# Kernel optimization log

Hardware: AMD Instinct MI355X
Metric: run time of the kernel (lower is better)

## Reference

```python
import jax, jax.numpy as jnp
import numpy as np
from jax import lax

EPS = 1e-5
B = 512

def _conv(x, w, pad):
    # x: [B,Cin,H,W], w: [Cout,Cin,kh,kw]
    return lax.conv_general_dilated(x, w, (1, 1), [(pad, pad), (pad, pad)],
                                    dimension_numbers=('NCHW', 'OIHW', 'NCHW'))

def _bn2d(x, g, b, m, v):
    s = g * lax.rsqrt(v + EPS)
    return x * s[None, :, None, None] + (b - m * s)[None, :, None, None]

def _bn1d(x, g, b, m, v):
    s = g * lax.rsqrt(v + EPS)
    return x * s + (b - m * s)

def _pool2(x):
    return lax.reduce_window(x, -jnp.inf, lax.max, (1, 1, 2, 2), (1, 1, 2, 2), 'VALID')

def setup_inputs() -> dict:
    key = jax.random.key(0)
    ks = iter(jax.random.split(key, 64))
    rn = lambda shape, s=1.0: jax.random.normal(next(ks), shape, dtype=jnp.float32) * s
    un = lambda shape: jax.random.uniform(next(ks), shape, dtype=jnp.float32, minval=0.5, maxval=1.5)
    def bn_params(c):
        return (jnp.ones((c,), jnp.float32), jnp.zeros((c,), jnp.float32), rn((c,), 0.1), un((c,)))
    inp = {"x": rn((B, 3, 64, 64))}
    inp["w1"] = rn((32, 3, 5, 5), 0.1)
    inp["bn1_g"], inp["bn1_b"], inp["bn1_m"], inp["bn1_v"] = bn_params(32)
    inp["w2"] = rn((64, 32, 3, 3), 0.06)
    inp["bn2_g"], inp["bn2_b"], inp["bn2_m"], inp["bn2_v"] = bn_params(64)
    inp["w3"] = rn((128, 64, 3, 3), 0.04)
    inp["bn3_g"], inp["bn3_b"], inp["bn3_m"], inp["bn3_v"] = bn_params(128)
    inp["fc_w"] = rn((256, 8192), 0.01)
    inp["fc_b"] = jnp.zeros((256,), jnp.float32)
    inp["bnf_g"], inp["bnf_b"], inp["bnf_m"], inp["bnf_v"] = bn_params(256)
    inp["c_w1"] = rn((64, 256), 0.06)
    inp["c_b1"] = jnp.zeros((64,), jnp.float32)
    inp["bnc_g"], inp["bnc_b"], inp["bnc_m"], inp["bnc_v"] = bn_params(64)
    inp["c_w2"] = rn((1, 64), 0.1)
    inp["c_b2"] = jnp.zeros((1,), jnp.float32)
    inp["m_w1"] = rn((64, 256), 0.06)
    inp["m_b1"] = jnp.zeros((64,), jnp.float32)
    inp["bnm_g"], inp["bnm_b"], inp["bnm_m"], inp["bnm_v"] = bn_params(64)
    inp["m_w2"] = rn((1, 64), 0.1)
    inp["m_b2"] = jnp.zeros((1,), jnp.float32)
    return inp

def reference(x, w1, bn1_g, bn1_b, bn1_m, bn1_v,
              w2, bn2_g, bn2_b, bn2_m, bn2_v,
              w3, bn3_g, bn3_b, bn3_m, bn3_v,
              fc_w, fc_b, bnf_g, bnf_b, bnf_m, bnf_v,
              c_w1, c_b1, bnc_g, bnc_b, bnc_m, bnc_v, c_w2, c_b2,
              m_w1, m_b1, bnm_g, bnm_b, bnm_m, bnm_v, m_w2, m_b2):
    # Block 1: conv5x5(3->32) + BN + ReLU + maxpool2 -> [B,32,32,32]
    h = _pool2(jax.nn.relu(_bn2d(_conv(x, w1, 2), bn1_g, bn1_b, bn1_m, bn1_v)))
    # Block 2: conv3x3(32->64) + BN + ReLU + maxpool2 -> [B,64,16,16]
    h = _pool2(jax.nn.relu(_bn2d(_conv(h, w2, 1), bn2_g, bn2_b, bn2_m, bn2_v)))
    # Block 3: conv3x3(64->128) + BN + ReLU + maxpool2 + ToDense -> [B,128,8,8]
    h = _pool2(jax.nn.relu(_bn2d(_conv(h, w3, 1), bn3_g, bn3_b, bn3_m, bn3_v)))
    f = h.reshape(h.shape[0], -1)  # [B, 8192]
    s = jax.nn.relu(_bn1d(f @ fc_w.T + fc_b, bnf_g, bnf_b, bnf_m, bnf_v))  # [B,256]
    c = jax.nn.relu(_bn1d(s @ c_w1.T + c_b1, bnc_g, bnc_b, bnc_m, bnc_v)) @ c_w2.T + c_b2
    mo = jax.nn.relu(_bn1d(s @ m_w1.T + m_b1, bnm_g, bnm_b, bnm_m, bnm_v)) @ m_w2.T + m_b2
    return (c, mo)  # ([B,1], [B,1])
```

## Files before the change

### kernel.cpp

```cpp
#include <hip/hip_runtime.h>
#include <hip/hip_bf16.h>

#define EPS 1e-5f

typedef __attribute__((ext_vector_type(8))) short bf16x8;
typedef __attribute__((ext_vector_type(4))) float f32x4;

__device__ __forceinline__ ushort f2b(float f) {
    return __builtin_bit_cast(ushort, __float2bfloat16(f));
}
__device__ __forceinline__ bf16x8 ld_frag(const char* p) {
    return __builtin_bit_cast(bf16x8, *reinterpret_cast<const uint4*>(p));
}

__global__ __launch_bounds__(256) void k_prep(
    const float* __restrict__ w1, const float* __restrict__ w2,
    const float* __restrict__ w3, const float* __restrict__ fcw,
    ushort* __restrict__ w1p, ushort* __restrict__ w2p,
    ushort* __restrict__ w3p, ushort* __restrict__ fcwp)
{
    const int total = 5120 + 18432 + 73728 + 2097152;
    for (int i = blockIdx.x * 256 + threadIdx.x; i < total; i += gridDim.x * 256) {
        if (i < 5120) {
            const int ky = i >> 10, co = (i >> 5) & 31, k = i & 31;
            const int kx = k >> 2, ci = k & 3;
            float v = 0.f;
            if (kx < 5 && ci < 3) v = w1[((co * 3 + ci) * 5 + ky) * 5 + kx];
            w1p[i] = f2b(v);
        } else if (i < 5120 + 18432) {
            const int j = i - 5120;
            const int tap = j >> 11, co = (j >> 5) & 63, ci = j & 31;
            w2p[j] = f2b(w2[(co * 32 + ci) * 9 + tap]);
        } else if (i < 5120 + 18432 + 73728) {
            const int j = i - (5120 + 18432);
            const int tap = j >> 13, co = (j >> 6) & 127, ci = j & 63;
            w3p[j] = f2b(w3[(co * 64 + ci) * 9 + tap]);
        } else {
            const int j = i - (5120 + 18432 + 73728);
            const int jrow = j >> 13, kp = j & 8191;
            const int c = kp & 127, p = kp >> 7;
            fcwp[j] = f2b(fcw[jrow * 8192 + c * 64 + p]);
        }
    }
}

__global__ __launch_bounds__(256) void k_conv1(
    const float* __restrict__ x, const ushort* __restrict__ w1p,
    const float* __restrict__ bg, const float* __restrict__ bb,
    const float* __restrict__ bm, const float* __restrict__ bv,
    ushort* __restrict__ h1)
{
    __shared__ __align__(16) ushort xs[12 * 72 * 4];
    __shared__ __align__(16) ushort ws[5 * 32 * 32];
    const int bid = blockIdx.x;
    const int n = bid >> 3, q = bid & 7;
    const int t = threadIdx.x;
    const int wave = t >> 6, lane = t & 63;
    const int g = lane >> 4, l15 = lane & 15;

    for (int idx = t; idx < 864; idx += 256) {
        const int row = idx / 72, col = idx - row * 72;
        const int gr = 8 * q - 2 + row, gc = col - 2;
        ushort p0 = 0, p1 = 0, p2 = 0;
        if ((unsigned)gr < 64u && (unsigned)gc < 64u) {
            const size_t base = ((size_t)n * 3 << 12) + (gr << 6) + gc;
            p0 = f2b(x[base]); p1 = f2b(x[base + 4096]); p2 = f2b(x[base + 8192]);
        }
        ushort4 pk; pk.x = p0; pk.y = p1; pk.z = p2; pk.w = 0;
        *reinterpret_cast<ushort4*>(&xs[idx * 4]) = pk;
    }
    for (int i = t; i < 640; i += 256) {
        const int gg = i & 3, r = i >> 2;
        const int co = r & 31;
        const uint4 v = *reinterpret_cast<const uint4*>(&w1p[r * 32 + gg * 8]);
        *reinterpret_cast<uint4*>((char*)ws + r * 64 + ((gg ^ ((co >> 1) & 3)) << 4)) = v;
    }
    __syncthreads();

    f32x4 acc[8][2];
    #pragma unroll
    for (int i = 0; i < 8; ++i) { acc[i][0] = (f32x4){0,0,0,0}; acc[i][1] = (f32x4){0,0,0,0}; }

    const char* xsb = (const char*)xs;
    const char* wsb = (const char*)ws;
    #pragma unroll
    for (int ky = 0; ky < 5; ++ky) {
        bf16x8 a[8], b[2];
        #pragma unroll
        for (int mt = 0; mt < 8; ++mt) {
            const int crl = 2 * wave + (mt >> 2);
            const int ccl = (mt & 3) * 16 + l15;
            const int off = ((crl + ky) * 72 + ccl) * 8 + g * 16;
            const uint2 lo = *reinterpret_cast<const uint2*>(xsb + off);
            const uint2 hi = *reinterpret_cast<const uint2*>(xsb + off + 8);
            uint4 all; all.x = lo.x; all.y = lo.y; all.z = hi.x; all.w = hi.y;
            a[mt] = __builtin_bit_cast(bf16x8, all);
        }
        #pragma unroll
        for (int nt = 0; nt < 2; ++nt) {
            const int co = nt * 16 + l15;
            b[nt] = ld_frag(wsb + (ky * 32 + co) * 64 + ((g ^ ((co >> 1) & 3)) << 4));
        }
        #pragma unroll
        for (int mt = 0; mt < 8; ++mt)
            #pragma unroll
            for (int nt = 0; nt < 2; ++nt)
                acc[mt][nt] = __builtin_amdgcn_mfma_f32_16x16x32_bf16(a[mt], b[nt], acc[mt][nt], 0, 0, 0);
    }

    const int prow = q * 4 + wave;
    #pragma unroll
    for (int nt = 0; nt < 2; ++nt) {
        const int co = nt * 16 + l15;
        const float s = bg[co] * rsqrtf(bv[co] + EPS);
        const float bsv = bb[co] - bm[co] * s;
        #pragma unroll
        for (int mt = 0; mt < 4; ++mt) {
            #pragma unroll
            for (int j = 0; j < 2; ++j) {
                const float v0 = fmaxf(fmaf(acc[mt][nt][2 * j],     s, bsv), 0.f);
                const float v1 = fmaxf(fmaf(acc[mt][nt][2 * j + 1], s, bsv), 0.f);
                const float v2 = fmaxf(fmaf(acc[mt + 4][nt][2 * j],     s, bsv), 0.f);
                const float v3 = fmaxf(fmaf(acc[mt + 4][nt][2 * j + 1], s, bsv), 0.f);
                const int ppc = mt * 8 + g * 2 + j;
                h1[(((size_t)n * 32 + prow) * 32 + ppc) * 32 + co] =
                    f2b(fmaxf(fmaxf(v0, v1), fmaxf(v2, v3)));
            }
        }
    }
}

__global__ __launch_bounds__(256) void k_conv2(
    const ushort* __restrict__ h1, const ushort* __restrict__ w2p,
    const float* __restrict__ bg, const float* __restrict__ bb,
    const float* __restrict__ bm, const float* __restrict__ bv,
    ushort* __restrict__ h2)
{
    __shared__ __align__(16) ushort xs[10 * 34 * 32];
    __shared__ __align__(16) ushort ws[9 * 64 * 32];
    const int bid = blockIdx.x;
    const int n = bid >> 2, q = bid & 3;
    const int t = threadIdx.x;
    const int wave = t >> 6, lane = t & 63;
    const int g = lane >> 4, l15 = lane & 15;

    for (int i = t; i < 1360; i += 256) {
        const int gg = i & 3, pix = i >> 2;
        const int row = pix / 34, col = pix - row * 34;
        const int gr = 8 * q - 1 + row, gc = col - 1;
        uint4 v = {0, 0, 0, 0};
        if ((unsigned)gr < 32u && (unsigned)gc < 32u)
            v = *reinterpret_cast<const uint4*>(&h1[((((size_t)n * 32 + gr) * 32 + gc) << 5) + gg * 8]);
        *reinterpret_cast<uint4*>((char*)xs + pix * 64 + ((gg ^ ((pix >> 1) & 3)) << 4)) = v;
    }
    for (int i = t; i < 2304; i += 256) {
        const int gg = i & 3, r = i >> 2;
        const int co = r & 63;
        const uint4 v = *reinterpret_cast<const uint4*>(&w2p[r * 32 + gg * 8]);
        *reinterpret_cast<uint4*>((char*)ws + r * 64 + ((gg ^ ((co >> 1) & 3)) << 4)) = v;
    }
    __syncthreads();

    f32x4 acc[4][4];
    #pragma unroll
    for (int i = 0; i < 4; ++i)
        #pragma unroll
        for (int j = 0; j < 4; ++j) acc[i][j] = (f32x4){0,0,0,0};

    const char* xsb = (const char*)xs;
    const char* wsb = (const char*)ws;
    #pragma unroll
    for (int tap = 0; tap < 9; ++tap) {
        const int ky = tap / 3, kx = tap - 3 * ky;
        bf16x8 a[4], b[4];
        #pragma unroll
        for (int mt = 0; mt < 4; ++mt) {
            const int crl = 2 * wave + (mt >> 1);
            const int ccl = (mt & 1) * 16 + l15;
            const int pix = (crl + ky) * 34 + ccl + kx;
            a[mt] = ld_frag(xsb + pix * 64 + ((g ^ ((pix >> 1) & 3)) << 4));
        }
        #pragma unroll
        for (int nt = 0; nt < 4; ++nt) {
            const int co = nt * 16 + l15;
            b[nt] = ld_frag(wsb + (tap * 64 + co) * 64 + ((g ^ ((co >> 1) & 3)) << 4));
        }
        #pragma unroll
        for (int mt = 0; mt < 4; ++mt)
            #pragma unroll
            for (int nt = 0; nt < 4; ++nt)
                acc[mt][nt] = __builtin_amdgcn_mfma_f32_16x16x32_bf16(a[mt], b[nt], acc[mt][nt], 0, 0, 0);
    }
    __syncthreads();

    const int prow = q * 4 + wave;
    #pragma unroll
    for (int nt = 0; nt < 4; ++nt) {
        const int co = nt * 16 + l15;
        const float s = bg[co] * rsqrtf(bv[co] + EPS);
        const float bsv = bb[co] - bm[co] * s;
        #pragma unroll
        for (int mtl = 0; mtl < 2; ++mtl) {
            #pragma unroll
            for (int j = 0; j < 2; ++j) {
                const float v0 = fmaxf(fmaf(acc[mtl][nt][2 * j],     s, bsv), 0.f);
                const float v1 = fmaxf(fmaf(acc[mtl][nt][2 * j + 1], s, bsv), 0.f);
                const float v2 = fmaxf(fmaf(acc[mtl + 2][nt][2 * j],     s, bsv), 0.f);
                const float v3 = fmaxf(fmaf(acc[mtl + 2][nt][2 * j + 1], s, bsv), 0.f);
                const int ppc = mtl * 8 + g * 2 + j;
                h2[(((size_t)n * 16 + prow) * 16 + ppc) * 64 + co] =
                    f2b(fmaxf(fmaxf(v0, v1), fmaxf(v2, v3)));
            }
        }
    }
}

__global__ __launch_bounds__(256) void k_conv3(
    const ushort* __restrict__ h2, const ushort* __restrict__ w3p,
    const float* __restrict__ bg, const float* __restrict__ bb,
    const float* __restrict__ bm, const float* __restrict__ bv,
    ushort* __restrict__ h3)
{
    __shared__ __align__(16) ushort xs[18 * 18 * 32];
    __shared__ __align__(16) ushort ws[9 * 64 * 32];
    const int bid = blockIdx.x;
    const int n = bid >> 1, ch = bid & 1;
    const int t = threadIdx.x;
    const int wave = t >> 6, lane = t & 63;
    const int g = lane >> 4, l15 = lane & 15;

    f32x4 acc[4][4];
    #pragma unroll
    for (int i = 0; i < 4; ++i)
        #pragma unroll
        for (int j = 0; j < 4; ++j) acc[i][j] = (f32x4){0,0,0,0};

    const char* xsb = (const char*)xs;
    const char* wsb = (const char*)ws;

    for (int gci = 0; gci < 2; ++gci) {
        if (gci) __syncthreads();
        for (int i = t; i < 1296; i += 256) {
            const int gg = i & 3, pix = i >> 2;
            const int row = pix / 18, col = pix - row * 18;
            const int gr = row - 1, gc = col - 1;
            uint4 v = {0, 0, 0, 0};
            if ((unsigned)gr < 16u && (unsigned)gc < 16u)
                v = *reinterpret_cast<const uint4*>(
                    &h2[((((size_t)n * 16 + gr) * 16 + gc) << 6) + gci * 32 + gg * 8]);
            *reinterpret_cast<uint4*>((char*)xs + pix * 64 + ((gg ^ ((pix >> 1) & 3)) << 4)) = v;
        }
        for (int i = t; i < 2304; i += 256) {
            const int gg = i & 3, r = i >> 2;
            const int tap = r >> 6, co = r & 63;
            const uint4 v = *reinterpret_cast<const uint4*>(
                &w3p[((size_t)(tap * 128 + ch * 64 + co) << 6) + gci * 32 + gg * 8]);
            *reinterpret_cast<uint4*>((char*)ws + r * 64 + ((gg ^ ((co >> 1) & 3)) << 4)) = v;
        }
        __syncthreads();
        #pragma unroll
        for (int tap = 0; tap < 9; ++tap) {
            const int ky = tap / 3, kx = tap - 3 * ky;
            bf16x8 a[4], b[4];
            #pragma unroll
            for (int mt = 0; mt < 4; ++mt) {
                const int pr = 4 * wave + mt;
                const int pix = (pr + ky) * 18 + l15 + kx;
                a[mt] = ld_frag(xsb + pix * 64 + ((g ^ ((pix >> 1) & 3)) << 4));
            }
            #pragma unroll
            for (int nt = 0; nt < 4; ++nt) {
                const int co = nt * 16 + l15;
                b[nt] = ld_frag(wsb + (tap * 64 + co) * 64 + ((g ^ ((co >> 1) & 3)) << 4));
            }
            #pragma unroll
            for (int mt = 0; mt < 4; ++mt)
                #pragma unroll
                for (int nt = 0; nt < 4; ++nt)
                    acc[mt][nt] = __builtin_amdgcn_mfma_f32_16x16x32_bf16(a[mt], b[nt], acc[mt][nt], 0, 0, 0);
        }
    }

    #pragma unroll
    for (int nt = 0; nt < 4; ++nt) {
        const int co = ch * 64 + nt * 16 + l15;
        const float s = bg[co] * rsqrtf(bv[co] + EPS);
        const float bsv = bb[co] - bm[co] * s;
        #pragma unroll
        for (int mtl = 0; mtl < 2; ++mtl) {
            #pragma unroll
            for (int j = 0; j < 2; ++j) {
                const int mt = mtl * 2;
                const float v0 = fmaxf(fmaf(acc[mt][nt][2 * j],     s, bsv), 0.f);
                const float v1 = fmaxf(fmaf(acc[mt][nt][2 * j + 1], s, bsv), 0.f);
                const float v2 = fmaxf(fmaf(acc[mt + 1][nt][2 * j],     s, bsv), 0.f);
                const float v3 = fmaxf(fmaf(acc[mt + 1][nt][2 * j + 1], s, bsv), 0.f);
                const int ppr = 2 * wave + mtl;
                const int ppc = g * 2 + j;
                h3[(((size_t)n * 8 + ppr) * 8 + ppc) * 128 + co] =
                    f2b(fmaxf(fmaxf(v0, v1), fmaxf(v2, v3)));
            }
        }
    }
}

__global__ __launch_bounds__(512) void k_fc(
    const ushort* __restrict__ A, const ushort* __restrict__ Bw, float* __restrict__ C)
{
    __shared__ __align__(16) ushort As[256 * 32];
    __shared__ __align__(16) ushort Bs[128 * 32];
    const int bm = blockIdx.x, bn = blockIdx.y, kz = blockIdx.z;
    const int t = threadIdx.x;
    const int wave = t >> 6, lane = t & 63;
    const int wm = wave >> 1, wn = wave & 1;
    const int g = lane >> 4, l15 = lane & 15;

    f32x4 acc[4][4];
    #pragma unroll
    for (int i = 0; i < 4; ++i)
        #pragma unroll
        for (int j = 0; j < 4; ++j) acc[i][j] = (f32x4){0,0,0,0};

    const char* asb = (const char*)As;
    const char* bsb = (const char*)Bs;
    for (int kk = 0; kk < 32; ++kk) {
        const int k0 = kz * 1024 + kk * 32;
        if (kk) __syncthreads();
        for (int i = t; i < 1536; i += 512) {
            const int gg = i & 3, row = (i >> 2);
            if (row < 256) {
                const uint4 v = *reinterpret_cast<const uint4*>(
                    &A[(size_t)(bm * 256 + row) * 8192 + k0 + gg * 8]);
                *reinterpret_cast<uint4*>((char*)As + row * 64 + ((gg ^ ((row >> 1) & 3)) << 4)) = v;
            } else {
                const int rw = row - 256;
                const uint4 v = *reinterpret_cast<const uint4*>(
                    &Bw[(size_t)(bn * 128 + rw) * 8192 + k0 + gg * 8]);
                *reinterpret_cast<uint4*>((char*)Bs + rw * 64 + ((gg ^ ((rw >> 1) & 3)) << 4)) = v;
            }
        }
        __syncthreads();
        bf16x8 a[4], b[4];
        #pragma unroll
        for (int mt = 0; mt < 4; ++mt) {
            const int r = wm * 64 + mt * 16 + l15;
            a[mt] = ld_frag(asb + r * 64 + ((g ^ ((r >> 1) & 3)) << 4));
        }
        #pragma unroll
        for (int nt = 0; nt < 4; ++nt) {
            const int r = wn * 64 + nt * 16 + l15;
            b[nt] = ld_frag(bsb + r * 64 + ((g ^ ((r >> 1) & 3)) << 4));
        }
        #pragma unroll
        for (int mt = 0; mt < 4; ++mt)
            #pragma unroll
            for (int nt = 0; nt < 4; ++nt)
                acc[mt][nt] = __builtin_amdgcn_mfma_f32_16x16x32_bf16(a[mt], b[nt], acc[mt][nt], 0, 0, 0);
    }

    #pragma unroll
    for (int mt = 0; mt < 4; ++mt) {
        #pragma unroll
        for (int nt = 0; nt < 4; ++nt) {
            const int col = bn * 128 + wn * 64 + nt * 16 + l15;
            #pragma unroll
            for (int r = 0; r < 4; ++r) {
                const int row = bm * 256 + wm * 64 + mt * 16 + g * 4 + r;
                atomicAdd(&C[(size_t)row * 256 + col], acc[mt][nt][r]);
            }
        }
    }
}

__global__ __launch_bounds__(128) void k_heads(
    const float* __restrict__ sraw, const float* __restrict__ fcb,
    const float* __restrict__ fg, const float* __restrict__ fb,
    const float* __restrict__ fm, const float* __restrict__ fv,
    const float* __restrict__ cw1, const float* __restrict__ cb1,
    const float* __restrict__ cg, const float* __restrict__ cbb,
    const float* __restrict__ cm, const float* __restrict__ cv,
    const float* __restrict__ cw2, const float* __restrict__ cb2,
    const float* __restrict__ mw1, const float* __restrict__ mb1,
    const float* __restrict__ mg, const float* __restrict__ mbb,
    const float* __restrict__ mm, const float* __restrict__ mv,
    const float* __restrict__ mw2, const float* __restrict__ mb2,
    float* __restrict__ outp)
{
    __shared__ float sv[256];
    const int b = blockIdx.x, t = threadIdx.x;
    for (int k = t; k < 256; k += 128) {
        const float val = sraw[b * 256 + k] + fcb[k];
        const float s = fg[k] * rsqrtf(fv[k] + EPS);
        sv[k] = fmaxf(fmaf(val, s, fb[k] - fm[k] * s), 0.f);
    }
    __syncthreads();
    const int j = t & 63;
    const bool isM = (t >= 64);
    const float* w1  = isM ? mw1 : cw1;
    const float* b1  = isM ? mb1 : cb1;
    const float* g1  = isM ? mg  : cg;
    const float* bb1 = isM ? mbb : cbb;
    const float* m1  = isM ? mm  : cm;
    const float* v1  = isM ? mv  : cv;
    const float* w2  = isM ? mw2 : cw2;
    const float* b2  = isM ? mb2 : cb2;
    float d = 0.f;
    const float* wr = w1 + j * 256;
    #pragma unroll 8
    for (int k = 0; k < 256; ++k) d = fmaf(sv[k], wr[k], d);
    d += b1[j];
    const float s1 = g1[j] * rsqrtf(v1[j] + EPS);
    d = fmaxf(fmaf(d, s1, bb1[j] - m1[j] * s1), 0.f);
    float prod = d * w2[j];
    #pragma unroll
    for (int off = 32; off > 0; off >>= 1) prod += __shfl_down(prod, off);
    if (j == 0) outp[(isM ? 512 : 0) + b] = prod + b2[0];
}

extern "C" void kernel_launch(void* const* d_in, const int* in_sizes, int n_in,
                              void* d_out, int out_size, void* d_ws, size_t ws_size,
                              hipStream_t stream)
{
    const float* x    = (const float*)d_in[0];
    const float* w1   = (const float*)d_in[1];
    const float* bn1g = (const float*)d_in[2];
    const float* bn1b = (const float*)d_in[3];
    const float* bn1m = (const float*)d_in[4];
    const float* bn1v = (const float*)d_in[5];
    const float* w2   = (const float*)d_in[6];
    const float* bn2g = (const float*)d_in[7];
    const float* bn2b = (const float*)d_in[8];
    const float* bn2m = (const float*)d_in[9];
    const float* bn2v = (const float*)d_in[10];
    const float* w3   = (const float*)d_in[11];
    const float* bn3g = (const float*)d_in[12];
    const float* bn3b = (const float*)d_in[13];
    const float* bn3m = (const float*)d_in[14];
    const float* bn3v = (const float*)d_in[15];
    const float* fcw  = (const float*)d_in[16];
    const float* fcb  = (const float*)d_in[17];
    const float* bnfg = (const float*)d_in[18];
    const float* bnfb = (const float*)d_in[19];
    const float* bnfm = (const float*)d_in[20];
    const float* bnfv = (const float*)d_in[21];
    const float* cw1  = (const float*)d_in[22];
    const float* cb1  = (const float*)d_in[23];
    const float* bncg = (const float*)d_in[24];
    const float* bncb = (const float*)d_in[25];
    const float* bncm = (const float*)d_in[26];
    const float* bncv = (const float*)d_in[27];
    const float* cw2  = (const float*)d_in[28];
    const float* cb2  = (const float*)d_in[29];
    const float* mw1  = (const float*)d_in[30];
    const float* mb1  = (const float*)d_in[31];
    const float* bnmg = (const float*)d_in[32];
    const float* bnmb = (const float*)d_in[33];
    const float* bnmm = (const float*)d_in[34];
    const float* bnmv = (const float*)d_in[35];
    const float* mw2  = (const float*)d_in[36];
    const float* mb2  = (const float*)d_in[37];

    char* W = (char*)d_ws;
    ushort* h1   = (ushort*)(W);
    ushort* h2   = (ushort*)(W + 33554432);
    ushort* h3   = (ushort*)(W + 50331648);
    float*  sr   = (float*) (W + 58720256);
    ushort* w1p  = (ushort*)(W + 59244544);
    ushort* w2p  = (ushort*)(W + 59254784);
    ushort* w3p  = (ushort*)(W + 59291648);
    ushort* fcwp = (ushort*)(W + 59439104);
    float* outp = (float*)d_out;

    k_prep<<<2048, 256, 0, stream>>>(w1, w2, w3, fcw, w1p, w2p, w3p, fcwp);
    k_conv1<<<512 * 8, 256, 0, stream>>>(x, w1p, bn1g, bn1b, bn1m, bn1v, h1);
    k_conv2<<<512 * 4, 256, 0, stream>>>(h1, w2p, bn2g, bn2b, bn2m, bn2v, h2);
    k_conv3<<<512 * 2, 256, 0, stream>>>(h2, w3p, bn3g, bn3b, bn3m, bn3v, h3);
    hipMemsetAsync(sr, 0, (size_t)512 * 256 * sizeof(float), stream);
    k_fc<<<dim3(2, 2, 8), 512, 0, stream>>>(h3, fcwp, sr);
    k_heads<<<512, 128, 0, stream>>>(sr, fcb, bnfg, bnfb, bnfm, bnfv,
                                     cw1, cb1, bncg, bncb, bncm, bncv, cw2, cb2,
                                     mw1, mb1, bnmg, bnmb, bnmm, bnmv, mw2, mb2, outp);
}
```

Baseline: 289.1 us.

## Split FC weight transpose into LDS kernel and retile FC GEMM with split-K partials

Moves the fc weight permutation and bf16 conversion into its own kernel, which stages each row through LDS so both the global reads and writes are coalesced. The FC GEMM shrinks its tile from 256x128 to 64x64 and raises split-K from 8 to 16, so the grid grows from 32 to 512 blocks and fills the GPU. Each split now writes plain partial sums into a separate buffer, which removes the atomics and the memset; the heads kernel adds the 16 partials. The costs are a 16x larger partial buffer, extra reads in the heads kernel, and lower operand reuse per block.

```diff
diff --git a/kernel.cpp b/kernel.cpp
--- a/kernel.cpp
+++ b/kernel.cpp
@@ -15,11 +15,10 @@
 
 __global__ __launch_bounds__(256) void k_prep(
     const float* __restrict__ w1, const float* __restrict__ w2,
-    const float* __restrict__ w3, const float* __restrict__ fcw,
-    ushort* __restrict__ w1p, ushort* __restrict__ w2p,
-    ushort* __restrict__ w3p, ushort* __restrict__ fcwp)
-{
-    const int total = 5120 + 18432 + 73728 + 2097152;
+    const float* __restrict__ w3,
+    ushort* __restrict__ w1p, ushort* __restrict__ w2p, ushort* __restrict__ w3p)
+{
+    const int total = 5120 + 18432 + 73728;
     for (int i = blockIdx.x * 256 + threadIdx.x; i < total; i += gridDim.x * 256) {
         if (i < 5120) {
             const int ky = i >> 10, co = (i >> 5) & 31, k = i & 31;
@@ -31,16 +30,33 @@
             const int j = i - 5120;
             const int tap = j >> 11, co = (j >> 5) & 63, ci = j & 31;
             w2p[j] = f2b(w2[(co * 32 + ci) * 9 + tap]);
-        } else if (i < 5120 + 18432 + 73728) {
+        } else {
             const int j = i - (5120 + 18432);
             const int tap = j >> 13, co = (j >> 6) & 127, ci = j & 63;
             w3p[j] = f2b(w3[(co * 64 + ci) * 9 + tap]);
-        } else {
-            const int j = i - (5120 + 18432 + 73728);
-            const int jrow = j >> 13, kp = j & 8191;
-            const int c = kp & 127, p = kp >> 7;
-            fcwp[j] = f2b(fcw[jrow * 8192 + c * 64 + p]);
-        }
+        }
+    }
+}
+
+__global__ __launch_bounds__(256) void k_prep_fc(
+    const float* __restrict__ fcw, ushort* __restrict__ fcwp)
+{
+    __shared__ ushort l[128 * 66];
+    const int j = blockIdx.x, t = threadIdx.x;
+    const float* src = fcw + (size_t)j * 8192;
+    #pragma unroll
+    for (int i = 0; i < 32; ++i) {
+        const int idx = i * 256 + t;
+        const int c = idx >> 6, p = idx & 63;
+        l[c * 66 + p] = f2b(src[idx]);
+    }
+    __syncthreads();
+    ushort* dst = fcwp + (size_t)j * 8192;
+    #pragma unroll
+    for (int i = 0; i < 32; ++i) {
+        const int idx = i * 256 + t;
+        const int c = idx & 127, p = idx >> 7;
+        dst[idx] = l[c * 66 + p];
     }
 }
 
@@ -304,70 +320,58 @@
     }
 }
 
-__global__ __launch_bounds__(512) void k_fc(
+__global__ __launch_bounds__(256) void k_fc(
     const ushort* __restrict__ A, const ushort* __restrict__ Bw, float* __restrict__ C)
 {
-    __shared__ __align__(16) ushort As[256 * 32];
-    __shared__ __align__(16) ushort Bs[128 * 32];
+    __shared__ __align__(16) ushort As[64 * 32];
+    __shared__ __align__(16) ushort Bs[64 * 32];
     const int bm = blockIdx.x, bn = blockIdx.y, kz = blockIdx.z;
     const int t = threadIdx.x;
     const int wave = t >> 6, lane = t & 63;
-    const int wm = wave >> 1, wn = wave & 1;
     const int g = lane >> 4, l15 = lane & 15;
 
-    f32x4 acc[4][4];
-    #pragma unroll
-    for (int i = 0; i < 4; ++i)
-        #pragma unroll
-        for (int j = 0; j < 4; ++j) acc[i][j] = (f32x4){0,0,0,0};
+    f32x4 acc[4];
+    #pragma unroll
+    for (int i = 0; i < 4; ++i) acc[i] = (f32x4){0,0,0,0};
 
     const char* asb = (const char*)As;
     const char* bsb = (const char*)Bs;
-    for (int kk = 0; kk < 32; ++kk) {
-        const int k0 = kz * 1024 + kk * 32;
+    for (int kk = 0; kk < 16; ++kk) {
+        const int k0 = kz * 512 + kk * 32;
         if (kk) __syncthreads();
-        for (int i = t; i < 1536; i += 512) {
-            const int gg = i & 3, row = (i >> 2);
-            if (row < 256) {
-                const uint4 v = *reinterpret_cast<const uint4*>(
-                    &A[(size_t)(bm * 256 + row) * 8192 + k0 + gg * 8]);
-                *reinterpret_cast<uint4*>((char*)As + row * 64 + ((gg ^ ((row >> 1) & 3)) << 4)) = v;
-            } else {
-                const int rw = row - 256;
-                const uint4 v = *reinterpret_cast<const uint4*>(
-                    &Bw[(size_t)(bn * 128 + rw) * 8192 + k0 + gg * 8]);
-                *reinterpret_cast<uint4*>((char*)Bs + rw * 64 + ((gg ^ ((rw >> 1) & 3)) << 4)) = v;
-            }
+        {
+            const int gg = t & 3, row = t >> 2;
+            const uint4 va = *reinterpret_cast<const uint4*>(
+                &A[(size_t)(bm * 64 + row) * 8192 + k0 + gg * 8]);
+            *reinterpret_cast<uint4*>((char*)As + row * 64 + ((gg ^ ((row >> 1) & 3)) << 4)) = va;
+            const uint4 vb = *reinterpret_cast<const uint4*>(
+                &Bw[(size_t)(bn * 64 + row) * 8192 + k0 + gg * 8]);
+            *reinterpret_cast<uint4*>((char*)Bs + row * 64 + ((gg ^ ((row >> 1) & 3)) << 4)) = vb;
         }
         __syncthreads();
-        bf16x8 a[4], b[4];
+        bf16x8 a[4], b;
         #pragma unroll
         for (int mt = 0; mt < 4; ++mt) {
-            const int r = wm * 64 + mt * 16 + l15;
+            const int r = mt * 16 + l15;
             a[mt] = ld_frag(asb + r * 64 + ((g ^ ((r >> 1) & 3)) << 4));
         }
-        #pragma unroll
-        for (int nt = 0; nt < 4; ++nt) {
-            const int r = wn * 64 + nt * 16 + l15;
-            b[nt] = ld_frag(bsb + r * 64 + ((g ^ ((r >> 1) & 3)) << 4));
+        {
+            const int r = wave * 16 + l15;
+            b = ld_frag(bsb + r * 64 + ((g ^ ((r >> 1) & 3)) << 4));
         }
         #pragma unroll
         for (int mt = 0; mt < 4; ++mt)
-            #pragma unroll
-            for (int nt = 0; nt < 4; ++nt)
-                acc[mt][nt] = __builtin_amdgcn_mfma_f32_16x16x32_bf16(a[mt], b[nt], acc[mt][nt], 0, 0, 0);
-    }
-
+            acc[mt] = __builtin_amdgcn_mfma_f32_16x16x32_bf16(a[mt], b, acc[mt], 0, 0, 0);
+    }
+
+    float* Cp = C + (size_t)kz * 512 * 256;
+    const int col = bn * 64 + wave * 16 + l15;
     #pragma unroll
     for (int mt = 0; mt < 4; ++mt) {
         #pragma unroll
-        for (int nt = 0; nt < 4; ++nt) {
-            const int col = bn * 128 + wn * 64 + nt * 16 + l15;
-            #pragma unroll
-            for (int r = 0; r < 4; ++r) {
-                const int row = bm * 256 + wm * 64 + mt * 16 + g * 4 + r;
-                atomicAdd(&C[(size_t)row * 256 + col], acc[mt][nt][r]);
-            }
+        for (int r = 0; r < 4; ++r) {
+            const int row = bm * 64 + mt * 16 + g * 4 + r;
+            Cp[(size_t)row * 256 + col] = acc[mt][r];
         }
     }
 }
@@ -389,7 +393,9 @@
     __shared__ float sv[256];
     const int b = blockIdx.x, t = threadIdx.x;
     for (int k = t; k < 256; k += 128) {
-        const float val = sraw[b * 256 + k] + fcb[k];
+        float val = fcb[k];
+        #pragma unroll
+        for (int z = 0; z < 16; ++z) val += sraw[(size_t)z * 131072 + b * 256 + k];
         const float s = fg[k] * rsqrtf(fv[k] + EPS);
         sv[k] = fmaxf(fmaf(val, s, fb[k] - fm[k] * s), 0.f);
     }
@@ -464,19 +470,19 @@
     ushort* h1   = (ushort*)(W);
     ushort* h2   = (ushort*)(W + 33554432);
     ushort* h3   = (ushort*)(W + 50331648);
-    float*  sr   = (float*) (W + 58720256);
-    ushort* w1p  = (ushort*)(W + 59244544);
-    ushort* w2p  = (ushort*)(W + 59254784);
-    ushort* w3p  = (ushort*)(W + 59291648);
-    ushort* fcwp = (ushort*)(W + 59439104);
+    ushort* w1p  = (ushort*)(W + 58720256);
+    ushort* w2p  = (ushort*)(W + 58730496);
+    ushort* w3p  = (ushort*)(W + 58767360);
+    ushort* fcwp = (ushort*)(W + 58914816);
+    float*  sr   = (float*) (W + 63109120);
     float* outp = (float*)d_out;
 
-    k_prep<<<2048, 256, 0, stream>>>(w1, w2, w3, fcw, w1p, w2p, w3p, fcwp);
+    k_prep<<<128, 256, 0, stream>>>(w1, w2, w3, w1p, w2p, w3p);
+    k_prep_fc<<<256, 256, 0, stream>>>(fcw, fcwp);
     k_conv1<<<512 * 8, 256, 0, stream>>>(x, w1p, bn1g, bn1b, bn1m, bn1v, h1);
     k_conv2<<<512 * 4, 256, 0, stream>>>(h1, w2p, bn2g, bn2b, bn2m, bn2v, h2);
     k_conv3<<<512 * 2, 256, 0, stream>>>(h2, w3p, bn3g, bn3b, bn3m, bn3v, h3);
-    hipMemsetAsync(sr, 0, (size_t)512 * 256 * sizeof(float), stream);
-    k_fc<<<dim3(2, 2, 8), 512, 0, stream>>>(h3, fcwp, sr);
+    k_fc<<<dim3(8, 4, 16), 256, 0, stream>>>(h3, fcwp, sr);
     k_heads<<<512, 128, 0, stream>>>(sr, fcb, bnfg, bnfb, bnfm, bnfv,
                                      cw1, cb1, bncg, bncb, bncm, bncv, cw2, cb2,
                                      mw1, mb1, bnmg, bnmb, bnmm, bnmv, mw2, mb2, outp);
```

After: 254.4 us. 12.0% less time.
